# Optimization experiments

Measured on AMD Instinct MI355X. Metric: run time of the kernel, lower is better.

## Reference

```python
import jax, jax.numpy as jnp
import numpy as np

N, E, CIN, CHID, DIM, KS = 6000, 192000, 32, 64, 3, 5
K = KS ** DIM          # 125 total spline kernel weights
S = 2 ** DIM           # 8 nonzero linear B-spline basis products per edge


def spline_conv(x, edge_index, pseudo, W, root, bias):
    """SplineConv, degree-1 open B-spline, mean aggregation, root weight + bias.
    x: [N, Cin], edge_index: [2, E], pseudo: [E, DIM] in [0,1],
    W: [K, Cin, Cout], root: [Cin, Cout], bias: [Cout].
    """
    src, dst = edge_index[0], edge_index[1]
    cin = x.shape[1]
    # open spline: KS-1 intervals over [0,1]
    u = pseudo * (KS - 1)                               # [E, DIM]
    i0 = jnp.clip(jnp.floor(u), 0, KS - 2).astype(jnp.int32)
    frac = u - i0                                       # [E, DIM]
    bits = (jnp.arange(S)[:, None] >> jnp.arange(DIM)[None, :]) & 1   # [S, DIM]
    strides = KS ** jnp.arange(DIM - 1, -1, -1)         # row-major flattening
    idx = jnp.sum((i0[:, None, :] + bits[None, :, :]) * strides, axis=-1)  # [E, S]
    basis = jnp.prod(jnp.where(bits[None, :, :] == 1,
                               frac[:, None, :], 1.0 - frac[:, None, :]), axis=-1)  # [E, S]
    x_j = x[src]                                        # gather: [E, Cin]
    vals = (basis[..., None] * x_j[:, None, :]).reshape(E * S, cin)
    keys = (dst[:, None] * K + idx).reshape(E * S)
    # bucket basis-weighted source features per (dst node, kernel index)
    T = jax.ops.segment_sum(vals, keys, num_segments=N * K).reshape(N, K, cin)
    out = jnp.einsum('nki,kio->no', T, W)               # [N, Cout]
    deg = jax.ops.segment_sum(jnp.ones((E,), jnp.float32), dst, num_segments=N)
    out = out / jnp.maximum(deg, 1.0)[:, None]          # mean aggregation
    return out + x @ root + bias


def _conv_params(key, cin):
    k1, k2 = jax.random.split(key)
    w_scale = 1.0 / np.sqrt(cin * S)
    W = jax.random.normal(k1, (K, cin, CHID), jnp.float32) * w_scale
    root = jax.random.normal(k2, (cin, CHID), jnp.float32) * (1.0 / np.sqrt(cin))
    b = jnp.zeros((CHID,), jnp.float32)
    return W, root, b


def setup_inputs() -> dict:
    key = jax.random.key(0)
    ks = jax.random.split(key, 10)
    inp = {
        'x': jax.random.normal(ks[0], (N, CIN), jnp.float32),
        'hidden': jax.random.normal(ks[1], (N, CHID), jnp.float32),
        'edge_index': jax.random.randint(ks[2], (2, E), 0, N, dtype=jnp.int32),
        'edge_attr': jax.random.uniform(ks[3], (E, DIM), jnp.float32),
    }
    for i, (name, cin) in enumerate([('xr', CIN), ('hr', CHID), ('xz', CIN),
                                     ('hz', CHID), ('xn', CIN), ('hn', CHID)]):
        W, root, b = _conv_params(ks[4 + i], cin)
        inp[f'W_{name}'] = W
        inp[f'root_{name}'] = root
        inp[f'b_{name}'] = b
    return inp


def reference(x, hidden, edge_index, edge_attr,
              W_xr, root_xr, b_xr, W_hr, root_hr, b_hr,
              W_xz, root_xz, b_xz, W_hz, root_hz, b_hz,
              W_xn, root_xn, b_xn, W_hn, root_hn, b_hn):
    hr_out = spline_conv(hidden, edge_index, edge_attr, W_hr, root_hr, b_hr)
    r = jax.nn.sigmoid(spline_conv(x, edge_index, edge_attr, W_xr, root_xr, b_xr) + hr_out)
    z = jax.nn.sigmoid(spline_conv(x, edge_index, edge_attr, W_xz, root_xz, b_xz)
                       + spline_conv(hidden, edge_index, edge_attr, W_hz, root_hz, b_hz))
    # NOTE: the original torch forward reuses self.hr (not self.hn) here; replicated faithfully.
    n = jnp.tanh(spline_conv(x, edge_index, edge_attr, W_xn, root_xn, b_xn) + r * hr_out)
    h_new = (1.0 - z) * n + z * hidden
    return h_new
```

## Files before the change

### kernel.cpp

```cpp
#include <hip/hip_runtime.h>
#include <math.h>

#define NN_   6000
#define EE_   192000
#define CIN_  32
#define CHID_ 64
#define KK_   125
#define EB_   32
#define CH1_  4
#define CH2_  8
#define CPB_  16
#define MTILE_ 192
#define DSTR_ 16

static __device__ __forceinline__ unsigned short f2bf(float f) {
    unsigned int u = __builtin_bit_cast(unsigned int, f);
    u += 0x7fff + ((u >> 16) & 1);
    return (unsigned short)(u >> 16);
}
static __device__ __forceinline__ float bf2f(unsigned short h) {
    unsigned int u = ((unsigned int)h) << 16;
    return __builtin_bit_cast(float, u);
}

template<int N> static __device__ __forceinline__ void vwait() {
    asm volatile("s_waitcnt vmcnt(%0)" :: "n"(N) : "memory");
    __builtin_amdgcn_sched_barrier(0);
}

#define PK1_ (192 * KK_ * CIN_)
#define PK2_ (128 * KK_ * CHID_)
#define CB_  ((EE_ + 255) / 256)
__global__ __launch_bounds__(256) void count_pack_kernel(
    const int* __restrict__ ei, int* __restrict__ deg,
    const float* __restrict__ W_xr, const float* __restrict__ W_xz,
    const float* __restrict__ W_xn, const float* __restrict__ W_hr,
    const float* __restrict__ W_hz,
    unsigned short* __restrict__ B1t, unsigned short* __restrict__ B2t)
{
    const int b = blockIdx.x;
    if (b < CB_) {
        int e = b * 256 + threadIdx.x;
        if (e < EE_) atomicAdd(&deg[ei[EE_ + e] * DSTR_], 1);
        return;
    }
    int gid = (b - CB_) * 256 + threadIdx.x;
    if (gid < PK1_) {
        int n  = gid / (KK_ * CIN_);
        int kk = gid % (KK_ * CIN_);
        int conv = n >> 6, o = n & 63;
        const float* W = (conv == 0) ? W_xr : ((conv == 1) ? W_xz : W_xn);
        B1t[gid] = f2bf(W[(size_t)kk * 64 + o]);
    } else if (gid < PK1_ + PK2_) {
        int g2 = gid - PK1_;
        int n  = g2 / (KK_ * CHID_);
        int kk = g2 % (KK_ * CHID_);
        int conv = n >> 6, o = n & 63;
        const float* W = (conv == 0) ? W_hr : W_hz;
        B2t[g2] = f2bf(W[(size_t)kk * 64 + o]);
    }
}

__global__ __launch_bounds__(1024) void scan_kernel(
    const int* __restrict__ deg, int* __restrict__ offs, int* __restrict__ cursor)
{
    __shared__ int part[1024];
    const int tid = threadIdx.x;
    const int CH = (NN_ + 1023) / 1024;
    const int base = tid * CH;
    int loc[CH];
    int s = 0;
#pragma unroll
    for (int i = 0; i < CH; ++i) {
        int v = (base + i < NN_) ? deg[(base + i) * DSTR_] : 0;
        loc[i] = s; s += v;
    }
    part[tid] = s;
    __syncthreads();
    for (int off = 1; off < 1024; off <<= 1) {
        int v = (tid >= off) ? part[tid - off] : 0;
        __syncthreads();
        part[tid] += v;
        __syncthreads();
    }
    const int pre = (tid > 0) ? part[tid - 1] : 0;
#pragma unroll
    for (int i = 0; i < CH; ++i) {
        if (base + i < NN_) {
            offs[base + i]            = pre + loc[i];
            cursor[(base + i) * DSTR_] = pre + loc[i];
        }
    }
    if (tid == 1023) offs[NN_] = part[1023];
}

__global__ __launch_bounds__(256) void prep_kernel(
    const int* __restrict__ ei, const float* __restrict__ attr,
    int* __restrict__ cursor, float4* __restrict__ meta_s, int* __restrict__ src_s)
{
    int e = blockIdx.x * 256 + threadIdx.x;
    if (e >= EE_) return;
    const int dst = ei[EE_ + e];
    const int p   = atomicAdd(&cursor[dst * DSTR_], 1);
    float f[3]; int i0[3];
#pragma unroll
    for (int d = 0; d < 3; ++d) {
        float u  = attr[e * 3 + d] * 4.0f;
        float fl = floorf(u);
        fl = fminf(fmaxf(fl, 0.0f), 3.0f);
        i0[d] = (int)fl;
        f[d]  = u - fl;
    }
    meta_s[p] = make_float4(f[0], f[1], f[2],
        __int_as_float(i0[0] * 25 + i0[1] * 5 + i0[2]));
    src_s[p] = ei[e];
}

template<int C>
__global__ __launch_bounds__(256) void build_T_kernel(
    const float4* __restrict__ meta_s, const int* __restrict__ src_s,
    const float* __restrict__ feat, const int* __restrict__ offs,
    unsigned short* __restrict__ Tb)
{
    constexpr int MP  = 40;
    constexpr int CT  = C / 16;
    constexpr int CPT = C / 8;
    using bf16x8 = __attribute__((ext_vector_type(8))) short;
    using f32x4  = __attribute__((ext_vector_type(4))) float;

    __shared__ __align__(16) unsigned short Mt [128 * MP];
    __shared__ __align__(16) unsigned short fbT[C   * MP];
    __shared__ int   s_src[EB_];
    __shared__ int   s_cell[EB_];
    __shared__ float s_basis[EB_ * 8];

    const int tid  = threadIdx.x;
    const int wave = tid >> 6;
    const int lane = tid & 63;
    const int quad = lane >> 4;
    const int l16  = lane & 15;
    const int node = blockIdx.x;

    for (int i = tid; i < C * MP / 8; i += 256)
        ((uint4*)fbT)[i] = make_uint4(0u, 0u, 0u, 0u);

    const int j0 = offs[node], j1 = offs[node + 1];

    f32x4 acc[2][CT];
#pragma unroll
    for (int t = 0; t < 2; ++t)
#pragma unroll
        for (int ct = 0; ct < CT; ++ct) acc[t][ct] = (f32x4){0.f, 0.f, 0.f, 0.f};

    for (int jb = j0; jb < j1; jb += EB_) {
        const int m = min(EB_, j1 - jb);

        __syncthreads();
        for (int i = tid; i < 128 * MP / 8; i += 256)
            ((uint4*)Mt)[i] = make_uint4(0u, 0u, 0u, 0u);
        if (tid < m) {
            const float4 mt = meta_s[jb + tid];
            s_src[tid]  = src_s[jb + tid];
            s_cell[tid] = __float_as_int(mt.w);
            const float f0 = mt.x, f1 = mt.y, f2 = mt.z;
            const float g0 = 1.f - f0, g1 = 1.f - f1, g2 = 1.f - f2;
            float4 blo = make_float4(g0*g1*g2, f0*g1*g2, g0*f1*g2, f0*f1*g2);
            float4 bhi = make_float4(g0*g1*f2, f0*g1*f2, g0*f1*f2, f0*f1*f2);
            *(float4*)&s_basis[tid * 8]     = blo;
            *(float4*)&s_basis[tid * 8 + 4] = bhi;
        }
        __syncthreads();

        {
            const int e = tid >> 3, s = tid & 7;
            if (e < m) {
                const int cell = s_cell[e] + 25 * (s & 1)
                               + 5 * ((s >> 1) & 1) + ((s >> 2) & 1);
                Mt[cell * MP + e] = f2bf(s_basis[e * 8 + s]);
            }
        }
        {
            const int e = tid >> 3, cg = (tid & 7) * CPT;
            if (e < m) {
                const float* fr = &feat[(size_t)s_src[e] * C + cg];
#pragma unroll
                for (int c4 = 0; c4 < CPT; c4 += 4) {
                    float4 v = *(const float4*)(fr + c4);
                    fbT[(cg + c4 + 0) * MP + e] = f2bf(v.x);
                    fbT[(cg + c4 + 1) * MP + e] = f2bf(v.y);
                    fbT[(cg + c4 + 2) * MP + e] = f2bf(v.z);
                    fbT[(cg + c4 + 3) * MP + e] = f2bf(v.w);
                }
            }
        }
        __syncthreads();

        bf16x8 a0 = *(const bf16x8*)&Mt[((wave * 2 + 0) * 16 + l16) * MP + quad * 8];
        bf16x8 a1 = *(const bf16x8*)&Mt[((wave * 2 + 1) * 16 + l16) * MP + quad * 8];
#pragma unroll
        for (int ct = 0; ct < CT; ++ct) {
            bf16x8 b = *(const bf16x8*)&fbT[(ct * 16 + l16) * MP + quad * 8];
            acc[0][ct] = __builtin_amdgcn_mfma_f32_16x16x32_bf16(a0, b, acc[0][ct], 0, 0, 0);
            acc[1][ct] = __builtin_amdgcn_mfma_f32_16x16x32_bf16(a1, b, acc[1][ct], 0, 0, 0);
        }
    }

    unsigned short* To = Tb + (size_t)node * (KK_ * C);
#pragma unroll
    for (int t = 0; t < 2; ++t) {
        const int rbase = (wave * 2 + t) * 16 + quad * 4;
#pragma unroll
        for (int ct = 0; ct < CT; ++ct) {
#pragma unroll
            for (int r = 0; r < 4; ++r) {
                const int R = rbase + r;
                if (R < KK_) To[R * C + ct * 16 + l16] = f2bf(acc[t][ct][r]);
            }
        }
    }
}

template<int NT, int NTF, int CPB, int LW>
static __device__ __forceinline__ void gemm_body(
    unsigned short* arena,
    const unsigned short* __restrict__ A, const unsigned short* __restrict__ Bt,
    const unsigned short* __restrict__ zp,
    unsigned short* __restrict__ P, int M, int Kd, int chunk, int zhalf)
{
    constexpr int COLS   = 64;
    constexpr int RF     = 3;
    constexpr int NFRAG  = NT / 16;
    constexpr int CSP    = NT + 8;
    constexpr int ASH    = MTILE_ * COLS;
    constexpr int SLOT   = ASH + 128 * COLS;
    constexpr int AUNITS = MTILE_ * COLS / 8;
    constexpr int BUNITS = NT * COLS / 8;

    using bf16x8 = __attribute__((ext_vector_type(8))) short;
    using f32x4  = __attribute__((ext_vector_type(4))) float;

    const int tid  = threadIdx.x;
    const int wave = tid >> 6;
    const int lane = tid & 63;
    const int quad = lane >> 4;
    const int l16  = lane & 15;
    const int m0   = blockIdx.x * MTILE_;
    const unsigned short* Bp = Bt + (size_t)zhalf * NT * Kd;
    const int kbase = chunk * CPB * COLS;
    const int ccmax = min(CPB, (Kd - kbase + COLS - 1) / COLS);

    f32x4 acc[RF][NFRAG];
#pragma unroll
    for (int t = 0; t < RF; ++t)
#pragma unroll
        for (int f = 0; f < NFRAG; ++f) acc[t][f] = (f32x4){0.f, 0.f, 0.f, 0.f};

    auto STAGE = [&](int cc, int slot) {
        unsigned short* Abuf = arena + slot * SLOT;
        unsigned short* Bbuf = Abuf + ASH;
        const int k0 = kbase + cc * COLS;
#pragma unroll
        for (int i = 0; i < AUNITS / 256; ++i) {
            const int u    = tid + i * 256;
            const int row  = u >> 3;
            const int gblk = (u & 7) ^ (row & 7);
            const int k    = k0 + gblk * 8;
            const unsigned short* g = (k + 8 <= Kd)
                ? A + (size_t)(m0 + row) * Kd + k
                : zp + (u & 3) * 8;
            __builtin_amdgcn_global_load_lds(
                (const __attribute__((address_space(1))) void*)g,
                (__attribute__((address_space(3))) void*)(Abuf + u * 8),
                16, 0, 0);
        }
#pragma unroll
        for (int i = 0; i < BUNITS / 256; ++i) {
            const int u    = tid + i * 256;
            const int row  = u >> 3;
            const int gblk = (u & 7) ^ (row & 7);
            const unsigned short* g = Bp + (size_t)row * Kd + k0 + gblk * 8;
            __builtin_amdgcn_global_load_lds(
                (const __attribute__((address_space(1))) void*)g,
                (__attribute__((address_space(3))) void*)(Bbuf + u * 8),
                16, 0, 0);
        }
    };

    STAGE(0, 0);

    for (int cc = 0; cc < ccmax; ++cc) {
        if (cc + 1 < ccmax) { STAGE(cc + 1, (cc + 1) & 1); vwait<LW>(); }
        else                { vwait<0>(); }
        __builtin_amdgcn_s_barrier();
        asm volatile("" ::: "memory");

        const unsigned short* Ac = arena + (cc & 1) * SLOT;
        const unsigned short* Bc = Ac + ASH;
        __builtin_amdgcn_s_setprio(1);
#pragma unroll
        for (int s = 0; s < 2; ++s) {
            bf16x8 av[RF];
#pragma unroll
            for (int t = 0; t < RF; ++t) {
                const int row = (wave * RF + t) * 16 + l16;
                av[t] = *(const bf16x8*)
                    &Ac[row * COLS + (((s * 4 + quad) ^ (l16 & 7)) * 8)];
            }
#pragma unroll
            for (int f = 0; f < NFRAG; ++f) {
                bf16x8 bv = *(const bf16x8*)
                    &Bc[(f * 16 + l16) * COLS + (((s * 4 + quad) ^ (l16 & 7)) * 8)];
#pragma unroll
                for (int t = 0; t < RF; ++t)
                    acc[t][f] = __builtin_amdgcn_mfma_f32_16x16x32_bf16(
                        av[t], bv, acc[t][f], 0, 0, 0);
            }
        }
        __builtin_amdgcn_s_setprio(0);
        asm volatile("" ::: "memory");
        __builtin_amdgcn_s_barrier();
        asm volatile("" ::: "memory");
    }

    unsigned short* Cs = arena;
    unsigned short* Pc = P + ((size_t)chunk * M + m0) * NTF + zhalf * NT;
#pragma unroll
    for (int p = 0; p < 3; ++p) {
        __syncthreads();
#pragma unroll
        for (int t = 0; t < RF; ++t) {
            const int fr = wave * RF + t;
            if ((fr >> 2) == p) {
                const int rb = (fr & 3) * 16 + quad * 4;
#pragma unroll
                for (int f = 0; f < NFRAG; ++f) {
                    const int col = f * 16 + l16;
#pragma unroll
                    for (int r = 0; r < 4; ++r)
                        Cs[(rb + r) * CSP + col] = f2bf(acc[t][f][r]);
                }
            }
        }
        __syncthreads();
        constexpr int UNITS = 64 * NT / 8;
        for (int u = tid; u < UNITS; u += 256) {
            const int row = (u * 8) / NT, col = (u * 8) % NT;
            if (m0 + p * 64 + row < M)
                *(uint4*)&Pc[(size_t)(p * 64 + row) * NTF + col] =
                    *(const uint4*)&Cs[row * CSP + col];
        }
    }
}

__global__ __launch_bounds__(256) void gemm_all_kernel(
    const unsigned short* __restrict__ Tx, const unsigned short* __restrict__ B1t,
    unsigned short* __restrict__ P1,
    const unsigned short* __restrict__ Th, const unsigned short* __restrict__ B2t,
    unsigned short* __restrict__ P2, const unsigned short* __restrict__ zp)
{
    __shared__ __align__(16) unsigned short arena[2 * 20480];
    const int y = blockIdx.y;
    if (y < CH2_) {
        gemm_body<128, 128, CPB_, 10>(arena, Th, B2t, zp, P2, NN_, KK_ * CHID_, y, 0);
    } else {
        const int g = y - CH2_;
        gemm_body<96, 192, CPB_, 9>(arena, Tx, B1t, zp, P1, NN_, KK_ * CIN_, g >> 1, g & 1);
    }
}

__global__ __launch_bounds__(256) void epilogue_kernel(
    const unsigned short* __restrict__ P1, const unsigned short* __restrict__ P2,
    const int* __restrict__ offs,
    const float* __restrict__ x, const float* __restrict__ hidden,
    const float* __restrict__ root_xr, const float* __restrict__ root_hr,
    const float* __restrict__ root_xz, const float* __restrict__ root_hz,
    const float* __restrict__ root_xn,
    const float* __restrict__ b_xr, const float* __restrict__ b_hr,
    const float* __restrict__ b_xz, const float* __restrict__ b_hz,
    const float* __restrict__ b_xn,
    float* __restrict__ out)
{
    __shared__ float xsh[4][32];
    __shared__ float hsh[4][64];
    const int w = threadIdx.x >> 6;
    const int o = threadIdx.x & 63;
    const int m = blockIdx.x * 4 + w;
    if (m >= NN_) return;

    if (o < 32) xsh[w][o] = x[(size_t)m * 32 + o];
    const float hval = hidden[(size_t)m * 64 + o];
    hsh[w][o] = hval;

    float axr = 0.f, axz = 0.f, axn = 0.f;
#pragma unroll
    for (int c = 0; c < CH1_; ++c) {
        const unsigned short* p = P1 + ((size_t)c * NN_ + m) * 192;
        axr += bf2f(p[o]); axz += bf2f(p[64 + o]); axn += bf2f(p[128 + o]);
    }
    float ahr = 0.f, ahz = 0.f;
#pragma unroll
    for (int c = 0; c < CH2_; ++c) {
        const unsigned short* p = P2 + ((size_t)c * NN_ + m) * 128;
        ahr += bf2f(p[o]); ahz += bf2f(p[64 + o]);
    }

    const int   dg   = offs[m + 1] - offs[m];
    const float dinv = 1.0f / fmaxf((float)dg, 1.0f);
    axr *= dinv; axz *= dinv; axn *= dinv; ahr *= dinv; ahz *= dinv;

    float sxr = 0.f, sxz = 0.f, sxn = 0.f;
#pragma unroll
    for (int c = 0; c < CIN_; ++c) {
        float xv = xsh[w][c];
        sxr += xv * root_xr[c * 64 + o];
        sxz += xv * root_xz[c * 64 + o];
        sxn += xv * root_xn[c * 64 + o];
    }
    float shr = 0.f, shz = 0.f;
#pragma unroll
    for (int c = 0; c < CHID_; ++c) {
        float hv = hsh[w][c];
        shr += hv * root_hr[c * 64 + o];
        shz += hv * root_hz[c * 64 + o];
    }

    const float conv_xr = axr + sxr + b_xr[o];
    const float conv_xz = axz + sxz + b_xz[o];
    const float conv_xn = axn + sxn + b_xn[o];
    const float hr_out  = ahr + shr + b_hr[o];
    const float conv_hz = ahz + shz + b_hz[o];

    const float rg = 1.0f / (1.0f + expf(-(conv_xr + hr_out)));
    const float zg = 1.0f / (1.0f + expf(-(conv_xz + conv_hz)));
    const float ng = tanhf(conv_xn + rg * hr_out);
    out[(size_t)m * 64 + o] = (1.0f - zg) * ng + zg * hval;
}

extern "C" void kernel_launch(void* const* d_in, const int* in_sizes, int n_in,
                              void* d_out, int out_size, void* d_ws, size_t ws_size,
                              hipStream_t stream)
{
    const float* x       = (const float*)d_in[0];
    const float* hidden  = (const float*)d_in[1];
    const int*   ei      = (const int*)  d_in[2];
    const float* attr    = (const float*)d_in[3];
    const float* W_xr    = (const float*)d_in[4];
    const float* root_xr = (const float*)d_in[5];
    const float* b_xr    = (const float*)d_in[6];
    const float* W_hr    = (const float*)d_in[7];
    const float* root_hr = (const float*)d_in[8];
    const float* b_hr    = (const float*)d_in[9];
    const float* W_xz    = (const float*)d_in[10];
    const float* root_xz = (const float*)d_in[11];
    const float* b_xz    = (const float*)d_in[12];
    const float* W_hz    = (const float*)d_in[13];
    const float* root_hz = (const float*)d_in[14];
    const float* b_hz    = (const float*)d_in[15];
    const float* W_xn    = (const float*)d_in[16];
    const float* root_xn = (const float*)d_in[17];
    const float* b_xn    = (const float*)d_in[18];
    float* out = (float*)d_out;

    char* w = (char*)d_ws;
    unsigned short* Tx  = (unsigned short*)w; w += (size_t)NN_ * KK_ * CIN_  * 2;
    unsigned short* Th  = (unsigned short*)w; w += (size_t)NN_ * KK_ * CHID_ * 2;
    unsigned short* B1t = (unsigned short*)w; w += (size_t)192 * KK_ * CIN_  * 2;
    unsigned short* B2t = (unsigned short*)w; w += (size_t)128 * KK_ * CHID_ * 2;
    unsigned short* P1  = (unsigned short*)w; w += (size_t)CH1_ * NN_ * 192 * 2;
    unsigned short* P2  = (unsigned short*)w; w += (size_t)CH2_ * NN_ * 128 * 2;
    float4* meta_s = (float4*)w; w += (size_t)EE_ * 16;
    int* src_s  = (int*)w;   w += (size_t)EE_ * 4;
    int* deg    = (int*)w;   w += (size_t)NN_ * DSTR_ * 4;
    int* offs   = (int*)w;   w += (size_t)(NN_ + 4) * 4;
    int* cursor = (int*)w;   w += (size_t)NN_ * DSTR_ * 4;
    unsigned short* zpad = (unsigned short*)w; w += 256;

    const int MT = (NN_ + MTILE_ - 1) / MTILE_;

    hipMemsetAsync(deg, 0, (size_t)NN_ * DSTR_ * 4, stream);
    hipMemsetAsync(zpad, 0, 256, stream);

    const int PACKB = (PK1_ + PK2_ + 255) / 256;
    count_pack_kernel<<<CB_ + PACKB, 256, 0, stream>>>(
        ei, deg, W_xr, W_xz, W_xn, W_hr, W_hz, B1t, B2t);

    scan_kernel<<<1, 1024, 0, stream>>>(deg, offs, cursor);
    prep_kernel<<<(EE_ + 255) / 256, 256, 0, stream>>>(ei, attr, cursor, meta_s, src_s);

    build_T_kernel<CHID_><<<NN_, 256, 0, stream>>>(meta_s, src_s, hidden, offs, Th);
    build_T_kernel<CIN_><<<NN_, 256, 0, stream>>>(meta_s, src_s, x, offs, Tx);

    gemm_all_kernel<<<dim3(MT, CH2_ + 2 * CH1_), 256, 0, stream>>>(
        Tx, B1t, P1, Th, B2t, P2, zpad);

    epilogue_kernel<<<(NN_ + 3) / 4, 256, 0, stream>>>(
        P1, P2, offs, x, hidden,
        root_xr, root_hr, root_xz, root_hz, root_xn,
        b_xr, b_hr, b_xz, b_hz, b_xn, out);
}
```

Before: 250.1 us.

## Widen build_T blocks to 512 threads, shrink GEMM M-tile, unpad degree arrays

The build_T kernel now runs 512 threads per node, so each wave owns one 16-row MFMA tile instead of two, and the basis scatter and the feature gather are done by separate halves of the block at the same time. The GEMM M-tile drops from 192 to 128 rows with fewer row fragments, smaller shared memory and a different pipeline-depth template argument, which gives more GEMM blocks. The degree and cursor arrays lose their 16-int padding stride, which makes them smaller but may bring back atomic contention between neighbouring counters.

Result: no change. 255.0 us (+2.0%).

```diff
diff --git a/kernel.cpp b/kernel.cpp
--- a/kernel.cpp
+++ b/kernel.cpp
@@ -10,8 +10,7 @@
 #define CH1_  4
 #define CH2_  8
 #define CPB_  16
-#define MTILE_ 192
-#define DSTR_ 16
+#define MTILE_ 128
 
 static __device__ __forceinline__ unsigned short f2bf(float f) {
     unsigned int u = __builtin_bit_cast(unsigned int, f);
@@ -41,7 +40,7 @@
     const int b = blockIdx.x;
     if (b < CB_) {
         int e = b * 256 + threadIdx.x;
-        if (e < EE_) atomicAdd(&deg[ei[EE_ + e] * DSTR_], 1);
+        if (e < EE_) atomicAdd(&deg[ei[EE_ + e]], 1);
         return;
     }
     int gid = (b - CB_) * 256 + threadIdx.x;
@@ -72,7 +71,7 @@
     int s = 0;
 #pragma unroll
     for (int i = 0; i < CH; ++i) {
-        int v = (base + i < NN_) ? deg[(base + i) * DSTR_] : 0;
+        int v = (base + i < NN_) ? deg[base + i] : 0;
         loc[i] = s; s += v;
     }
     part[tid] = s;
@@ -87,8 +86,8 @@
 #pragma unroll
     for (int i = 0; i < CH; ++i) {
         if (base + i < NN_) {
-            offs[base + i]            = pre + loc[i];
-            cursor[(base + i) * DSTR_] = pre + loc[i];
+            offs[base + i]   = pre + loc[i];
+            cursor[base + i] = pre + loc[i];
         }
     }
     if (tid == 1023) offs[NN_] = part[1023];
@@ -101,7 +100,7 @@
     int e = blockIdx.x * 256 + threadIdx.x;
     if (e >= EE_) return;
     const int dst = ei[EE_ + e];
-    const int p   = atomicAdd(&cursor[dst * DSTR_], 1);
+    const int p   = atomicAdd(&cursor[dst], 1);
     float f[3]; int i0[3];
 #pragma unroll
     for (int d = 0; d < 3; ++d) {
@@ -117,7 +116,7 @@
 }
 
 template<int C>
-__global__ __launch_bounds__(256) void build_T_kernel(
+__global__ __launch_bounds__(512) void build_T_kernel(
     const float4* __restrict__ meta_s, const int* __restrict__ src_s,
     const float* __restrict__ feat, const int* __restrict__ offs,
     unsigned short* __restrict__ Tb)
@@ -141,22 +140,20 @@
     const int l16  = lane & 15;
     const int node = blockIdx.x;
 
-    for (int i = tid; i < C * MP / 8; i += 256)
+    for (int i = tid; i < C * MP / 8; i += 512)
         ((uint4*)fbT)[i] = make_uint4(0u, 0u, 0u, 0u);
 
     const int j0 = offs[node], j1 = offs[node + 1];
 
-    f32x4 acc[2][CT];
-#pragma unroll
-    for (int t = 0; t < 2; ++t)
-#pragma unroll
-        for (int ct = 0; ct < CT; ++ct) acc[t][ct] = (f32x4){0.f, 0.f, 0.f, 0.f};
+    f32x4 acc[CT];
+#pragma unroll
+    for (int ct = 0; ct < CT; ++ct) acc[ct] = (f32x4){0.f, 0.f, 0.f, 0.f};
 
     for (int jb = j0; jb < j1; jb += EB_) {
         const int m = min(EB_, j1 - jb);
 
         __syncthreads();
-        for (int i = tid; i < 128 * MP / 8; i += 256)
+        for (int i = tid; i < 128 * MP / 8; i += 512)
             ((uint4*)Mt)[i] = make_uint4(0u, 0u, 0u, 0u);
         if (tid < m) {
             const float4 mt = meta_s[jb + tid];
@@ -171,16 +168,16 @@
         }
         __syncthreads();
 
-        {
+        if (tid < 256) {
             const int e = tid >> 3, s = tid & 7;
             if (e < m) {
                 const int cell = s_cell[e] + 25 * (s & 1)
                                + 5 * ((s >> 1) & 1) + ((s >> 2) & 1);
                 Mt[cell * MP + e] = f2bf(s_basis[e * 8 + s]);
             }
-        }
-        {
-            const int e = tid >> 3, cg = (tid & 7) * CPT;
+        } else {
+            const int u = tid - 256;
+            const int e = u >> 3, cg = (u & 7) * CPT;
             if (e < m) {
                 const float* fr = &feat[(size_t)s_src[e] * C + cg];
 #pragma unroll
@@ -195,27 +192,22 @@
         }
         __syncthreads();
 
-        bf16x8 a0 = *(const bf16x8*)&Mt[((wave * 2 + 0) * 16 + l16) * MP + quad * 8];
-        bf16x8 a1 = *(const bf16x8*)&Mt[((wave * 2 + 1) * 16 + l16) * MP + quad * 8];
+        bf16x8 a = *(const bf16x8*)&Mt[(wave * 16 + l16) * MP + quad * 8];
 #pragma unroll
         for (int ct = 0; ct < CT; ++ct) {
             bf16x8 b = *(const bf16x8*)&fbT[(ct * 16 + l16) * MP + quad * 8];
-            acc[0][ct] = __builtin_amdgcn_mfma_f32_16x16x32_bf16(a0, b, acc[0][ct], 0, 0, 0);
-            acc[1][ct] = __builtin_amdgcn_mfma_f32_16x16x32_bf16(a1, b, acc[1][ct], 0, 0, 0);
+            acc[ct] = __builtin_amdgcn_mfma_f32_16x16x32_bf16(a, b, acc[ct], 0, 0, 0);
         }
     }
 
     unsigned short* To = Tb + (size_t)node * (KK_ * C);
-#pragma unroll
-    for (int t = 0; t < 2; ++t) {
-        const int rbase = (wave * 2 + t) * 16 + quad * 4;
-#pragma unroll
-        for (int ct = 0; ct < CT; ++ct) {
-#pragma unroll
-            for (int r = 0; r < 4; ++r) {
-                const int R = rbase + r;
-                if (R < KK_) To[R * C + ct * 16 + l16] = f2bf(acc[t][ct][r]);
-            }
+    const int rbase = wave * 16 + quad * 4;
+#pragma unroll
+    for (int ct = 0; ct < CT; ++ct) {
+#pragma unroll
+        for (int r = 0; r < 4; ++r) {
+            const int R = rbase + r;
+            if (R < KK_) To[R * C + ct * 16 + l16] = f2bf(acc[ct][r]);
         }
     }
 }
@@ -228,13 +220,14 @@
     unsigned short* __restrict__ P, int M, int Kd, int chunk, int zhalf)
 {
     constexpr int COLS   = 64;
-    constexpr int RF     = 3;
+    constexpr int RF     = 2;
     constexpr int NFRAG  = NT / 16;
     constexpr int CSP    = NT + 8;
     constexpr int ASH    = MTILE_ * COLS;
     constexpr int SLOT   = ASH + 128 * COLS;
     constexpr int AUNITS = MTILE_ * COLS / 8;
     constexpr int BUNITS = NT * COLS / 8;
+    constexpr int NPASS  = MTILE_ / 64;
 
     using bf16x8 = __attribute__((ext_vector_type(8))) short;
     using f32x4  = __attribute__((ext_vector_type(4))) float;
@@ -325,7 +318,7 @@
     unsigned short* Cs = arena;
     unsigned short* Pc = P + ((size_t)chunk * M + m0) * NTF + zhalf * NT;
 #pragma unroll
-    for (int p = 0; p < 3; ++p) {
+    for (int p = 0; p < NPASS; ++p) {
         __syncthreads();
 #pragma unroll
         for (int t = 0; t < RF; ++t) {
@@ -358,13 +351,13 @@
     const unsigned short* __restrict__ Th, const unsigned short* __restrict__ B2t,
     unsigned short* __restrict__ P2, const unsigned short* __restrict__ zp)
 {
-    __shared__ __align__(16) unsigned short arena[2 * 20480];
+    __shared__ __align__(16) unsigned short arena[2 * 16384];
     const int y = blockIdx.y;
     if (y < CH2_) {
-        gemm_body<128, 128, CPB_, 10>(arena, Th, B2t, zp, P2, NN_, KK_ * CHID_, y, 0);
+        gemm_body<128, 128, CPB_, 8>(arena, Th, B2t, zp, P2, NN_, KK_ * CHID_, y, 0);
     } else {
         const int g = y - CH2_;
-        gemm_body<96, 192, CPB_, 9>(arena, Tx, B1t, zp, P1, NN_, KK_ * CIN_, g >> 1, g & 1);
+        gemm_body<96, 192, CPB_, 7>(arena, Tx, B1t, zp, P1, NN_, KK_ * CIN_, g >> 1, g & 1);
     }
 }
 
@@ -470,14 +463,14 @@
     unsigned short* P2  = (unsigned short*)w; w += (size_t)CH2_ * NN_ * 128 * 2;
     float4* meta_s = (float4*)w; w += (size_t)EE_ * 16;
     int* src_s  = (int*)w;   w += (size_t)EE_ * 4;
-    int* deg    = (int*)w;   w += (size_t)NN_ * DSTR_ * 4;
+    int* deg    = (int*)w;   w += (size_t)NN_ * 4;
     int* offs   = (int*)w;   w += (size_t)(NN_ + 4) * 4;
-    int* cursor = (int*)w;   w += (size_t)NN_ * DSTR_ * 4;
+    int* cursor = (int*)w;   w += (size_t)NN_ * 4;
     unsigned short* zpad = (unsigned short*)w; w += 256;
 
     const int MT = (NN_ + MTILE_ - 1) / MTILE_;
 
-    hipMemsetAsync(deg, 0, (size_t)NN_ * DSTR_ * 4, stream);
+    hipMemsetAsync(deg, 0, (size_t)NN_ * 4, stream);
     hipMemsetAsync(zpad, 0, 256, stream);
 
     const int PACKB = (PK1_ + PK2_ + 255) / 256;
@@ -487,8 +480,8 @@
     scan_kernel<<<1, 1024, 0, stream>>>(deg, offs, cursor);
     prep_kernel<<<(EE_ + 255) / 256, 256, 0, stream>>>(ei, attr, cursor, meta_s, src_s);
 
-    build_T_kernel<CHID_><<<NN_, 256, 0, stream>>>(meta_s, src_s, hidden, offs, Th);
-    build_T_kernel<CIN_><<<NN_, 256, 0, stream>>>(meta_s, src_s, x, offs, Tx);
+    build_T_kernel<CHID_><<<NN_, 512, 0, stream>>>(meta_s, src_s, hidden, offs, Th);
+    build_T_kernel<CIN_><<<NN_, 512, 0, stream>>>(meta_s, src_s, x, offs, Tx);
 
     gemm_all_kernel<<<dim3(MT, CH2_ + 2 * CH1_), 256, 0, stream>>>(
         Tx, B1t, P1, Th, B2t, P2, zpad);
```
